# Optimization experiments

Hardware: AMD Instinct MI355X
Metric: run time of the kernel (lower is better)

Reference implementation:

```python
import jax, jax.numpy as jnp
import numpy as np

B, T = 16, 512
LAT, ACT, TSK = 512, 64, 96
E, NH, HD = 1024, 16, 64
L, HID, MAXS = 4, 4096, 512


def setup_inputs() -> dict:
    key = jax.random.key(0)
    ks = jax.random.split(key, 16)
    def rn(k, shape, std=0.02):
        return jax.random.normal(k, shape, jnp.float32) * std
    return {
        "z": jax.random.normal(ks[0], (B, T, LAT), jnp.float32),
        "a": jax.random.normal(ks[1], (B, T, ACT), jnp.float32),
        "task_emb": jax.random.normal(ks[2], (B, T, TSK), jnp.float32),
        "input_proj_w": rn(ks[3], (LAT + ACT + TSK, E)),
        "input_proj_b": jnp.zeros((E,), jnp.float32),
        "pos_emb": rn(ks[4], (1, MAXS, E)),
        "ln1_w": jnp.ones((L, E), jnp.float32),
        "ln1_b": jnp.zeros((L, E), jnp.float32),
        "qkv_w": rn(ks[5], (L, E, 3 * E)),
        "proj_w": rn(ks[6], (L, E, E)),
        "proj_b": jnp.zeros((L, E), jnp.float32),
        "ln2_w": jnp.ones((L, E), jnp.float32),
        "ln2_b": jnp.zeros((L, E), jnp.float32),
        "mlp_w1": rn(ks[7], (L, E, HID)),
        "mlp_b1": jnp.zeros((L, HID), jnp.float32),
        "mlp_w2": rn(ks[8], (L, HID, E)),
        "mlp_b2": jnp.zeros((L, E), jnp.float32),
        "out_norm_w": jnp.ones((E,), jnp.float32),
        "out_norm_b": jnp.zeros((E,), jnp.float32),
        "delta_w": rn(ks[9], (E, LAT)),
        "delta_b": jnp.zeros((LAT,), jnp.float32),
    }


def _ln(x, w, b, eps=1e-5):
    mu = jnp.mean(x, -1, keepdims=True)
    var = jnp.mean((x - mu) ** 2, -1, keepdims=True)
    return (x - mu) * jax.lax.rsqrt(var + eps) * w + b


def reference(z, a, task_emb, input_proj_w, input_proj_b, pos_emb,
              ln1_w, ln1_b, qkv_w, proj_w, proj_b, ln2_w, ln2_b,
              mlp_w1, mlp_b1, mlp_w2, mlp_b2,
              out_norm_w, out_norm_b, delta_w, delta_b):
    Bv, Tv, _ = z.shape
    x = jnp.concatenate([z, a, task_emb], axis=-1) @ input_proj_w + input_proj_b
    x = x + pos_emb[:, :Tv]
    scale = HD ** -0.5
    causal = jnp.tril(jnp.ones((Tv, Tv), bool))  # seq_start=0, no cache
    for l in range(L):
        h = _ln(x, ln1_w[l], ln1_b[l])
        qkv = (h @ qkv_w[l]).reshape(Bv, Tv, 3, NH, HD)
        q = jnp.swapaxes(qkv[:, :, 0], 1, 2) * scale  # (B,H,T,D)
        k = jnp.swapaxes(qkv[:, :, 1], 1, 2)
        v = jnp.swapaxes(qkv[:, :, 2], 1, 2)
        attn = jnp.einsum('bhqd,bhkd->bhqk', q, k)
        attn = jnp.where(causal, attn, -jnp.inf)
        attn = jax.nn.softmax(attn, axis=-1)
        o = jnp.einsum('bhqk,bhkd->bhqd', attn, v)
        o = jnp.swapaxes(o, 1, 2).reshape(Bv, Tv, E)
        x = x + (o @ proj_w[l] + proj_b[l])
        h2 = _ln(x, ln2_w[l], ln2_b[l])
        mid = jax.nn.gelu(h2 @ mlp_w1[l] + mlp_b1[l], approximate=False)
        x = x + (mid @ mlp_w2[l] + mlp_b2[l])
    x = _ln(x, out_norm_w, out_norm_b)
    return z + (x @ delta_w + delta_b)
```

## Files before the change

kernel.cpp:

```cpp
#include <hip/hip_runtime.h>
#include <hip/hip_bf16.h>
#include <math.h>

typedef unsigned short u16;
typedef unsigned int u32;
typedef __attribute__((ext_vector_type(4))) float f32x4;
typedef __attribute__((ext_vector_type(8))) short bf16x8;

#define DEV static __device__ __forceinline__

DEV u16 f2bf(float f) {
  __hip_bfloat16 h = __float2bfloat16(f);
  union { __hip_bfloat16 h; u16 u; } c; c.h = h; return c.u;
}

DEV void gload16(const void* g, void* l) {
  __builtin_amdgcn_global_load_lds((const __attribute__((address_space(1))) u32*)g,
                                   (__attribute__((address_space(3))) u32*)l, 16, 0, 0);
}

__global__ void transpose_w(const float* __restrict__ src, u16* __restrict__ dst,
                            int R, int C, int Rp) {
  __shared__ float tile[32][33];
  int tx = threadIdx.x, ty = threadIdx.y;
  int c0 = blockIdx.x * 32, r0 = blockIdx.y * 32;
  #pragma unroll
  for (int j = 0; j < 4; j++) {
    int r = r0 + ty + j * 8, c = c0 + tx;
    tile[ty + j * 8][tx] = (r < R && c < C) ? src[(size_t)r * C + c] : 0.f;
  }
  __syncthreads();
  #pragma unroll
  for (int j = 0; j < 4; j++) {
    int cc = c0 + ty + j * 8;
    int rr = r0 + tx;
    if (cc < C && rr < Rp) dst[(size_t)cc * Rp + rr] = f2bf(tile[tx][ty + j * 8]);
  }
}

__global__ void concat_k(const float* __restrict__ z, const float* __restrict__ a,
                         const float* __restrict__ te, u16* __restrict__ A) {
  const int total = 8192 * 704;
  for (int idx = blockIdx.x * 256 + threadIdx.x; idx < total; idx += gridDim.x * 256) {
    int m = idx / 704;
    int j = idx - m * 704;
    float v = 0.f;
// ... 76 lines not shown
  for (int l = 0; l < LB; l++) {
    int c = l * 512 + tid, rw = c >> 2, g = (c & 3) ^ ((rw >> 1) & 3);
    boff[l] = rw * Krow + g * 16;
  }
  const int ra = wr * (FM * 16) + (lane & 15);
  const int aRd = ra * 64 + (((lane >> 4) ^ ((ra >> 1) & 3)) << 4);
  const int rb = wc * 64 + (lane & 15);
  const int bRd = rb * 64 + (((lane >> 4) ^ ((rb >> 1) & 3)) << 4);

  f32x4 zero4 = {0.f, 0.f, 0.f, 0.f};
  f32x4 acc[FM][4];
  #pragma unroll
  for (int m = 0; m < FM; m++)
    #pragma unroll
    for (int n = 0; n < 4; n++) acc[m][n] = zero4;

  auto stageA = [&](int s) {
    char* Ad = lds + (s & 3) * SLICE;
    const char* src = Ag + (size_t)s * 64;
    #pragma unroll
    for (int l = 0; l < LA; l++)
      gload16(src + aoff[l], Ad + (l * 512 + w * 64) * 16);
  };
  auto stageB = [&](int s) {
    char* Bd = lds + (s & 3) * SLICE + ABYTES;
    const char* src = Bg + (size_t)s * 64;
    #pragma unroll
    for (int l = 0; l < LB; l++)
      gload16(src + boff[l], Bd + (l * 512 + w * 64) * 16);
  };

  const int NS = K >> 5;
  stageA(0); stageB(0); stageA(1); stageB(1);
  if constexpr (FM == 8) asm volatile("s_waitcnt vmcnt(4)" ::: "memory");
  else                   asm volatile("s_waitcnt vmcnt(3)" ::: "memory");
  __builtin_amdgcn_s_barrier();

  #pragma unroll 1
  for (int s = 0; s < NS; s++) {
    char* Ar = lds + (s & 3) * SLICE;
    char* Br = Ar + ABYTES;
    const bool pre = (s + 2 < NS);
    bf16x8 bfr[4], af[4];
    if constexpr (FM == 8) {
      #pragma unroll
      for (int n = 0; n < 4; n++) bfr[n] = *(const bf16x8*)(Br + bRd + n * 1024);
      #pragma unroll
      for (int m = 0; m < 4; m++) af[m] = *(const bf16x8*)(Ar + aRd + m * 1024);
      if (pre) stageA(s + 2);
      __builtin_amdgcn_sched_barrier(0);
      __builtin_amdgcn_s_barrier();
      asm volatile("s_waitcnt lgkmcnt(0)" ::: "memory");
      __builtin_amdgcn_sched_barrier(0);
      __builtin_amdgcn_s_setprio(1);
      #pragma unroll
      for (int m = 0; m < 4; m++)
        #pragma unroll
        for (int n = 0; n < 4; n++)
          acc[m][n] = __builtin_amdgcn_mfma_f32_16x16x32_bf16(af[m], bfr[n], acc[m][n], 0, 0, 0);
      __builtin_amdgcn_s_setprio(0);
      __builtin_amdgcn_sched_barrier(0);
      __builtin_amdgcn_s_barrier();
      #pragma unroll
      for (int m = 0; m < 4; m++) af[m] = *(const bf16x8*)(Ar + aRd + 4096 + m * 1024);
      if (pre) stageB(s + 2);
      __builtin_amdgcn_sched_barrier(0);
      __builtin_amdgcn_s_barrier();
      asm volatile("s_waitcnt lgkmcnt(0)" ::: "memory");
      __builtin_amdgcn_sched_barrier(0);
      __builtin_amdgcn_s_setprio(1);
      #pragma unroll
      for (int m = 0; m < 4; m++)
        #pragma unroll
        for (int n = 0; n < 4; n++)
          acc[4 + m][n] = __builtin_amdgcn_mfma_f32_16x16x32_bf16(af[m], bfr[n], acc[4 + m][n], 0, 0, 0);
      __builtin_amdgcn_s_setprio(0);
      __builtin_amdgcn_sched_barrier(0);
      if (pre) asm volatile("s_waitcnt vmcnt(4)" ::: "memory");
      else     asm volatile("s_waitcnt vmcnt(0)" ::: "memory");
      __builtin_amdgcn_s_barrier();
    } else {
      #pragma unroll
      for (int n = 0; n < 4; n++) bfr[n] = *(const bf16x8*)(Br + bRd + n * 1024);
      #pragma unroll
      for (int m = 0; m < 4; m++) af[m] = *(const bf16x8*)(Ar + aRd + m * 1024);
      if (pre) { stageA(s + 2); stageB(s + 2); }
      __builtin_amdgcn_sched_barrier(0);
      __builtin_amdgcn_s_barrier();
      asm volatile("s_waitcnt lgkmcnt(0)" ::: "memory");
      __builtin_amdgcn_sched_barrier(0);
      __builtin_amdgcn_s_setprio(1);
      #pragma unroll
      for (int m = 0; m < 4; m++)
        #pragma unroll
        for (int n = 0; n < 4; n++)
          acc[m][n] = __builtin_amdgcn_mfma_f32_16x16x32_bf16(af[m], bfr[n], acc[m][n], 0, 0, 0);
      __builtin_amdgcn_s_setprio(0);
      __builtin_amdgcn_sched_barrier(0);
      if (pre) asm volatile("s_waitcnt vmcnt(3)" ::: "memory");
      else     asm volatile("s_waitcnt vmcnt(0)" ::: "memory");
      __builtin_amdgcn_s_barrier();
    }
  }

  #pragma unroll
  for (int m = 0; m < FM; m++) {
    #pragma unroll
    for (int i = 0; i < 4; i++) {
      int gm = m0 + wr * (FM * 16) + m * 16 + ((lane >> 4) << 2) + i;
      #pragma unroll
      for (int n = 0; n < 4; n++) {
        int gn = n0 + wc * 64 + n * 16 + (lane & 15);
        float v = acc[m][n][i];
        if (EPI & 1) v += bias[gn];
        if (EPI & 2) v += pos[(size_t)(gm & 511) * N + gn];
        if (EPI & 4) v += res[(size_t)gm * N + gn];
        if (EPI & 8) v = 0.5f * v * (1.f + erff(v * 0.70710678118654752f));
        if (EPI & 16) outH[(size_t)gm * N + gn] = f2bf(v);
        else outF[(size_t)gm * N + gn] = v;
      }
    }
  }
}

__global__ __launch_bounds__(512) void attn_k(const u16* __restrict__ qkv,
                                              u16* __restrict__ o) {
  __shared__ u16 Ks[512 * 64];
  __shared__ u16 Vt[64 * 512];
  __shared__ u16 Ps[8 * 512];
  const int tid = threadIdx.x, lane = tid & 63, w = tid >> 6;
  const int b = blockIdx.x >> 4, h = blockIdx.x & 15;
  const u16* base = qkv + (size_t)b * 512 * 3072 + h * 64;

  #pragma unroll
  for (int it = 0; it < 8; it++) {
    int chunk = it * 512 + tid;
    int row = chunk >> 3;
    int ib = (chunk & 7) * 16;
    int lb = ib ^ ((row & 7) << 4);
    gload16((const char*)(base + 1024 + (size_t)row * 3072) + lb,
            (char*)Ks + (it * 512 + w * 64) * 16);
  }
  {
    const u16* vrow = base + 2048 + (size_t)tid * 3072;
    #pragma unroll
    for (int c = 0; c < 8; c++) {
      uint4 u = *(const uint4*)(vrow + c * 8);
      u32 vals[4] = {u.x, u.y, u.z, u.w};
      #pragma unroll
      for (int pcompo = 0; pcompo < 4; pcompo++) {
        int d0 = c * 8 + pcompo * 2;
        size_t by0 = ((size_t)d0 * 1024 + tid * 2) ^ (size_t)((d0 & 7) << 4);
        size_t by1 = ((size_t)(d0 + 1) * 1024 + tid * 2) ^ (size_t)(((d0 + 1) & 7) << 4);
        *(u16*)((char*)Vt + by0) = (u16)(vals[pcompo] & 0xffff);
        *(u16*)((char*)Vt + by1) = (u16)(vals[pcompo] >> 16);
      }
// ... 132 lines not shown
  };
  u16* wt_in   = (u16*)alloc((size_t)1024 * 704 * 2);
  u16* wt_qkv  = (u16*)alloc((size_t)4 * 3072 * 1024 * 2);
  u16* wt_proj = (u16*)alloc((size_t)4 * 1024 * 1024 * 2);
  u16* wt_m1   = (u16*)alloc((size_t)4 * 4096 * 1024 * 2);
  u16* wt_m2   = (u16*)alloc((size_t)4 * 1024 * 4096 * 2);
  u16* wt_d    = (u16*)alloc((size_t)512 * 1024 * 2);
  u16* abuf    = (u16*)alloc((size_t)8192 * 704 * 2);
  float* xbuf  = (float*)alloc((size_t)8192 * 1024 * 4);
  u16* hbuf    = (u16*)alloc((size_t)8192 * 1024 * 2);
  u16* big     = (u16*)alloc((size_t)8192 * 4096 * 2);
  u16* obuf    = (u16*)alloc((size_t)8192 * 1024 * 2);
  u16* qkvb = big;
  u16* mid  = big;

  dim3 tb(32, 8);
  auto TR = [&](const float* s, u16* d, int R, int C, int Rp) {
    dim3 g((C + 31) / 32, (Rp + 31) / 32);
    transpose_w<<<g, tb, 0, stream>>>(s, d, R, C, Rp);
  };
  TR(ipw, wt_in, 672, 1024, 704);
  for (int l = 0; l < 4; l++) TR(qkvw + (size_t)l * 1024 * 3072, wt_qkv + (size_t)l * 3072 * 1024, 1024, 3072, 1024);
  for (int l = 0; l < 4; l++) TR(projw + (size_t)l * 1024 * 1024, wt_proj + (size_t)l * 1024 * 1024, 1024, 1024, 1024);
  for (int l = 0; l < 4; l++) TR(w1 + (size_t)l * 1024 * 4096, wt_m1 + (size_t)l * 4096 * 1024, 1024, 4096, 1024);
  for (int l = 0; l < 4; l++) TR(w2 + (size_t)l * 4096 * 1024, wt_m2 + (size_t)l * 1024 * 4096, 4096, 1024, 4096);
  TR(dw, wt_d, 1024, 512, 1024);

  concat_k<<<4096, 256, 0, stream>>>(z, a, te, abuf);

  gemm8<4, 3><<<4 * 64, 512, 0, stream>>>(abuf, wt_in, xbuf, nullptr, ipb, nullptr, pos, 8192, 1024, 704, 4);

  for (int l = 0; l < 4; l++) {
    ln_k<<<2048, 256, 0, stream>>>(xbuf, ln1w + l * 1024, ln1b + l * 1024, hbuf);
    gemm8<8, 16><<<12 * 32, 512, 0, stream>>>(hbuf, wt_qkv + (size_t)l * 3072 * 1024, nullptr, qkvb, nullptr, nullptr, nullptr, 8192, 3072, 1024, 12);
    attn_k<<<256, 512, 0, stream>>>(qkvb, obuf);
    gemm8<4, 5><<<4 * 64, 512, 0, stream>>>(obuf, wt_proj + (size_t)l * 1024 * 1024, xbuf, nullptr, projb + l * 1024, xbuf, nullptr, 8192, 1024, 1024, 4);
    ln_k<<<2048, 256, 0, stream>>>(xbuf, ln2w + l * 1024, ln2b + l * 1024, hbuf);
    gemm8<8, 25><<<16 * 32, 512, 0, stream>>>(hbuf, wt_m1 + (size_t)l * 4096 * 1024, nullptr, mid, b1 + l * 4096, nullptr, nullptr, 8192, 4096, 1024, 16);
    gemm8<4, 5><<<4 * 64, 512, 0, stream>>>(mid, wt_m2 + (size_t)l * 1024 * 4096, xbuf, nullptr, b2 + l * 1024, xbuf, nullptr, 8192, 1024, 4096, 4);
  }
  ln_k<<<2048, 256, 0, stream>>>(xbuf, onw, onb, hbuf);
  gemm8<4, 5><<<2 * 64, 512, 0, stream>>>(hbuf, wt_d, out, nullptr, db, z, nullptr, 8192, 512, 1024, 2);
}
```

Baseline: 1.548 ms.

## Add new pipelined GEMM kernel with K-halved stages and XCD-aware tile mapping

Adds a gemmP kernel that splits each 64-wide K tile into two 32-wide halves in double-buffered LDS. It interleaves LDS reads, global-to-LDS prefetches and MFMA phases at a finer grain, and remaps block IDs so that consecutive tiles land on the same XCD. All the main transformer GEMMs now use this kernel, and gemm8 is reduced to its FM=4 path, which only the input projection still uses. The aim is to hide global load latency better and improve L2 locality. In exchange it adds more barriers per K step and uses a larger LDS footprint, which may lower occupancy.

```diff
diff --git a/kernel.cpp b/kernel.cpp
--- a/kernel.cpp
+++ b/kernel.cpp
@@ -154,8 +154,7 @@
 
   const int NS = K >> 5;
   stageA(0); stageB(0); stageA(1); stageB(1);
-  if constexpr (FM == 8) asm volatile("s_waitcnt vmcnt(4)" ::: "memory");
-  else                   asm volatile("s_waitcnt vmcnt(3)" ::: "memory");
+  asm volatile("s_waitcnt vmcnt(3)" ::: "memory");
   __builtin_amdgcn_s_barrier();
 
   #pragma unroll 1
@@ -164,65 +163,26 @@
     char* Br = Ar + ABYTES;
     const bool pre = (s + 2 < NS);
     bf16x8 bfr[4], af[4];
-    if constexpr (FM == 8) {
-      #pragma unroll
-      for (int n = 0; n < 4; n++) bfr[n] = *(const bf16x8*)(Br + bRd + n * 1024);
-      #pragma unroll
-      for (int m = 0; m < 4; m++) af[m] = *(const bf16x8*)(Ar + aRd + m * 1024);
-      if (pre) stageA(s + 2);
-      __builtin_amdgcn_sched_barrier(0);
-      __builtin_amdgcn_s_barrier();
-      asm volatile("s_waitcnt lgkmcnt(0)" ::: "memory");
-      __builtin_amdgcn_sched_barrier(0);
-      __builtin_amdgcn_s_setprio(1);
-      #pragma unroll
-      for (int m = 0; m < 4; m++)
-        #pragma unroll
-        for (int n = 0; n < 4; n++)
-          acc[m][n] = __builtin_amdgcn_mfma_f32_16x16x32_bf16(af[m], bfr[n], acc[m][n], 0, 0, 0);
-      __builtin_amdgcn_s_setprio(0);
-      __builtin_amdgcn_sched_barrier(0);
-      __builtin_amdgcn_s_barrier();
-      #pragma unroll
-      for (int m = 0; m < 4; m++) af[m] = *(const bf16x8*)(Ar + aRd + 4096 + m * 1024);
-      if (pre) stageB(s + 2);
-      __builtin_amdgcn_sched_barrier(0);
-      __builtin_amdgcn_s_barrier();
-      asm volatile("s_waitcnt lgkmcnt(0)" ::: "memory");
-      __builtin_amdgcn_sched_barrier(0);
-      __builtin_amdgcn_s_setprio(1);
-      #pragma unroll
-      for (int m = 0; m < 4; m++)
-        #pragma unroll
-        for (int n = 0; n < 4; n++)
-          acc[4 + m][n] = __builtin_amdgcn_mfma_f32_16x16x32_bf16(af[m], bfr[n], acc[4 + m][n], 0, 0, 0);
-      __builtin_amdgcn_s_setprio(0);
-      __builtin_amdgcn_sched_barrier(0);
-      if (pre) asm volatile("s_waitcnt vmcnt(4)" ::: "memory");
-      else     asm volatile("s_waitcnt vmcnt(0)" ::: "memory");
-      __builtin_amdgcn_s_barrier();
-    } else {
-      #pragma unroll
-      for (int n = 0; n < 4; n++) bfr[n] = *(const bf16x8*)(Br + bRd + n * 1024);
-      #pragma unroll
-      for (int m = 0; m < 4; m++) af[m] = *(const bf16x8*)(Ar + aRd + m * 1024);
-      if (pre) { stageA(s + 2); stageB(s + 2); }
-      __builtin_amdgcn_sched_barrier(0);
-      __builtin_amdgcn_s_barrier();
-      asm volatile("s_waitcnt lgkmcnt(0)" ::: "memory");
-      __builtin_amdgcn_sched_barrier(0);
-      __builtin_amdgcn_s_setprio(1);
-      #pragma unroll
-      for (int m = 0; m < 4; m++)
-        #pragma unroll
-        for (int n = 0; n < 4; n++)
-          acc[m][n] = __builtin_amdgcn_mfma_f32_16x16x32_bf16(af[m], bfr[n], acc[m][n], 0, 0, 0);
-      __builtin_amdgcn_s_setprio(0);
-      __builtin_amdgcn_sched_barrier(0);
-      if (pre) asm volatile("s_waitcnt vmcnt(3)" ::: "memory");
-      else     asm volatile("s_waitcnt vmcnt(0)" ::: "memory");
-      __builtin_amdgcn_s_barrier();
-    }
+    #pragma unroll
+    for (int n = 0; n < 4; n++) bfr[n] = *(const bf16x8*)(Br + bRd + n * 1024);
+    #pragma unroll
+    for (int m = 0; m < 4; m++) af[m] = *(const bf16x8*)(Ar + aRd + m * 1024);
+    if (pre) { stageA(s + 2); stageB(s + 2); }
+    __builtin_amdgcn_sched_barrier(0);
+    __builtin_amdgcn_s_barrier();
+    asm volatile("s_waitcnt lgkmcnt(0)" ::: "memory");
+    __builtin_amdgcn_sched_barrier(0);
+    __builtin_amdgcn_s_setprio(1);
+    #pragma unroll
+    for (int m = 0; m < 4; m++)
+      #pragma unroll
+      for (int n = 0; n < 4; n++)
+        acc[m][n] = __builtin_amdgcn_mfma_f32_16x16x32_bf16(af[m], bfr[n], acc[m][n], 0, 0, 0);
+    __builtin_amdgcn_s_setprio(0);
+    __builtin_amdgcn_sched_barrier(0);
+    if (pre) asm volatile("s_waitcnt vmcnt(3)" ::: "memory");
+    else     asm volatile("s_waitcnt vmcnt(0)" ::: "memory");
+    __builtin_amdgcn_s_barrier();
   }
 
   #pragma unroll
@@ -244,6 +204,198 @@
     }
   }
 }
+
+#define PHASE_MID \
+  __builtin_amdgcn_sched_barrier(0); \
+  __builtin_amdgcn_s_barrier(); \
+  asm volatile("s_waitcnt lgkmcnt(0)" ::: "memory"); \
+  __builtin_amdgcn_sched_barrier(0); \
+  __builtin_amdgcn_s_setprio(1);
+
+#define PHASE_END \
+  __builtin_amdgcn_s_setprio(0); \
+  __builtin_amdgcn_sched_barrier(0); \
+  __builtin_amdgcn_s_barrier();
+
+template <int FM, int EPI>
+__global__ __launch_bounds__(512, 2) void gemmP(
+    const u16* __restrict__ A, const u16* __restrict__ BT,
+    float* __restrict__ outF, u16* __restrict__ outH,
+    const float* __restrict__ bias, const float* __restrict__ res,
+    const float* __restrict__ pos, int M, int N, int K, int gx) {
+  constexpr int BM = FM * 32;
+  constexpr int ARB = BM * 64;
+  constexpr int BRB = 256 * 64;
+  constexpr int ABYT = 4 * ARB;
+  constexpr int LA = BM / 128;
+  __shared__ char lds[ABYT + 4 * BRB];
+
+  const int tid = threadIdx.x, lane = tid & 63, w = tid >> 6;
+  const int wr = w >> 2, wc = w & 3;
+
+  const int nwg = gridDim.x, orig = blockIdx.x;
+  const int q = nwg >> 3, r = nwg & 7;
+  const int xcd = orig & 7, loc = orig >> 3;
+  const int sid = (xcd < r ? xcd * (q + 1) : r * (q + 1) + (xcd - r) * q) + loc;
+  const int m0 = (sid / gx) * BM, n0 = (sid % gx) * 256;
+
+  const char* Ag = (const char*)(A + (size_t)m0 * K);
+  const char* Bg = (const char*)(BT + (size_t)n0 * K);
+  const int K2 = K * 2;
+  const int NT = K >> 6, NTm1 = NT - 1, NI = NT >> 1;
+
+  int aRd[FM], bRd[4];
+  #pragma unroll
+  for (int m = 0; m < FM; m++) {
+    int rr = wr * (FM * 16) + m * 16 + (lane & 15);
+    aRd[m] = rr * 64 + (((lane >> 4) ^ ((rr >> 1) & 3)) << 4);
+  }
+  #pragma unroll
+  for (int n = 0; n < 4; n++) {
+    int rr = wc * 64 + n * 16 + (lane & 15);
+    bRd[n] = rr * 64 + (((lane >> 4) ^ ((rr >> 1) & 3)) << 4);
+  }
+  int asrc[LA], adst[LA], bsrc[2], bdst[2];
+  #pragma unroll
+  for (int l = 0; l < LA; l++) {
+    int c = l * 512 + tid, rw = c >> 2, sl = c & 3;
+    asrc[l] = rw * K2 + ((sl ^ ((rw >> 1) & 3)) << 4);
+    adst[l] = c * 16;
+  }
+  #pragma unroll
+  for (int l = 0; l < 2; l++) {
+    int c = l * 512 + tid, rw = c >> 2, sl = c & 3;
+    bsrc[l] = rw * K2 + ((sl ^ ((rw >> 1) & 3)) << 4);
+    bdst[l] = c * 16;
+  }
+
+  auto stA = [&](int tau, int kh) {
+    char* d = lds + ((tau & 1) * 2 + kh) * ARB;
+    const char* s = Ag + (size_t)(tau < NT ? tau : NTm1) * 128 + kh * 64;
+    #pragma unroll
+    for (int l = 0; l < LA; l++) gload16(s + asrc[l], d + adst[l]);
+  };
+  auto stB = [&](int tau, int kh) {
+    char* d = lds + ABYT + ((tau & 1) * 2 + kh) * BRB;
+    const char* s = Bg + (size_t)(tau < NT ? tau : NTm1) * 128 + kh * 64;
+    #pragma unroll
+    for (int l = 0; l < 2; l++) gload16(s + bsrc[l], d + bdst[l]);
+  };
+
+  f32x4 zero4 = {0.f, 0.f, 0.f, 0.f};
+  f32x4 acc[FM][4];
+  #pragma unroll
+  for (int m = 0; m < FM; m++)
+    #pragma unroll
+    for (int n = 0; n < 4; n++) acc[m][n] = zero4;
+
+  bf16x8 afr[4], bfr[4];
+  auto rdA4 = [&](int buf, int kh, int mb) {
+    const char* base = lds + (buf * 2 + kh) * ARB;
+    #pragma unroll
+    for (int mm = 0; mm < 4; mm++) afr[mm] = *(const bf16x8*)(base + aRd[mb + mm]);
+  };
+  auto rdB4 = [&](int buf, int kh) {
+    const char* base = lds + ABYT + (buf * 2 + kh) * BRB;
+    #pragma unroll
+    for (int nn = 0; nn < 4; nn++) bfr[nn] = *(const bf16x8*)(base + bRd[nn]);
+  };
+
+#define MFMA16(MB) \
+  _Pragma("unroll") \
+  for (int mm = 0; mm < 4; mm++) \
+    _Pragma("unroll") \
+    for (int nn = 0; nn < 4; nn++) \
+      acc[(MB) + mm][nn] = __builtin_amdgcn_mfma_f32_16x16x32_bf16(afr[mm], bfr[nn], acc[(MB) + mm][nn], 0, 0, 0);
+
+  if constexpr (FM == 8) {
+    stA(0, 0); stB(0, 0); stA(0, 1); stB(0, 1); stA(1, 0); stB(1, 0); stB(1, 1);
+    asm volatile("s_waitcnt vmcnt(8)" ::: "memory");
+  } else {
+    stA(0, 0); stB(0, 0); stA(0, 1); stB(0, 1); stA(1, 0); stB(1, 0);
+    asm volatile("s_waitcnt vmcnt(3)" ::: "memory");
+  }
+  __builtin_amdgcn_s_barrier();
+
+  #pragma unroll 1
+  for (int J = 0; J < NI; J++) {
+    const int t = 2 * J;
+    if constexpr (FM == 8) {
+      asm volatile("s_waitcnt vmcnt(8)" ::: "memory");
+      __builtin_amdgcn_sched_barrier(0);
+      rdB4(0, 0); rdA4(0, 0, 0); stA(t + 1, 1);
+      PHASE_MID; MFMA16(0); PHASE_END;
+      asm volatile("s_waitcnt vmcnt(8)" ::: "memory");
+      __builtin_amdgcn_sched_barrier(0);
+      rdA4(0, 0, 4); stB(t + 2, 0);
+      PHASE_MID; MFMA16(4); PHASE_END;
+      asm volatile("s_waitcnt vmcnt(8)" ::: "memory");
+      __builtin_amdgcn_sched_barrier(0);
+      rdB4(0, 1); rdA4(0, 1, 0); stA(t + 2, 0);
+      PHASE_MID; MFMA16(0); PHASE_END;
+      asm volatile("s_waitcnt vmcnt(8)" ::: "memory");
+      __builtin_amdgcn_sched_barrier(0);
+      rdA4(0, 1, 4); stB(t + 2, 1);
+      PHASE_MID; MFMA16(4); PHASE_END;
+      asm volatile("s_waitcnt vmcnt(8)" ::: "memory");
+      __builtin_amdgcn_sched_barrier(0);
+      rdB4(1, 0); rdA4(1, 0, 0); stA(t + 2, 1);
+      PHASE_MID; MFMA16(0); PHASE_END;
+      asm volatile("s_waitcnt vmcnt(8)" ::: "memory");
+      __builtin_amdgcn_sched_barrier(0);
+      rdA4(1, 0, 4); stB(t + 3, 0);
+      PHASE_MID; MFMA16(4); PHASE_END;
+      asm volatile("s_waitcnt vmcnt(8)" ::: "memory");
+      __builtin_amdgcn_sched_barrier(0);
+      rdB4(1, 1); rdA4(1, 1, 0); stA(t + 3, 0);
+      PHASE_MID; MFMA16(0); PHASE_END;
+      asm volatile("s_waitcnt vmcnt(8)" ::: "memory");
+      __builtin_amdgcn_sched_barrier(0);
+      rdA4(1, 1, 4); stB(t + 3, 1);
+      PHASE_MID; MFMA16(4); PHASE_END;
+    } else {
+      asm volatile("s_waitcnt vmcnt(3)" ::: "memory");
+      __builtin_amdgcn_sched_barrier(0);
+      rdB4(0, 0); rdA4(0, 0, 0); stA(t + 1, 1); stB(t + 1, 1);
+      PHASE_MID; MFMA16(0); PHASE_END;
+      asm volatile("s_waitcnt vmcnt(3)" ::: "memory");
+      __builtin_amdgcn_sched_barrier(0);
+      rdB4(0, 1); rdA4(0, 1, 0); stA(t + 2, 0); stB(t + 2, 0);
+      PHASE_MID; MFMA16(0); PHASE_END;
+      asm volatile("s_waitcnt vmcnt(3)" ::: "memory");
+      __builtin_amdgcn_sched_barrier(0);
+      rdB4(1, 0); rdA4(1, 0, 0); stA(t + 2, 1); stB(t + 2, 1);
+      PHASE_MID; MFMA16(0); PHASE_END;
+      asm volatile("s_waitcnt vmcnt(3)" ::: "memory");
+      __builtin_amdgcn_sched_barrier(0);
+      rdB4(1, 1); rdA4(1, 1, 0); stA(t + 3, 0); stB(t + 3, 0);
+      PHASE_MID; MFMA16(0); PHASE_END;
+    }
+  }
+  asm volatile("s_waitcnt vmcnt(0)" ::: "memory");
+
+  #pragma unroll
+  for (int m = 0; m < FM; m++) {
+    #pragma unroll
+    for (int i = 0; i < 4; i++) {
+      int gm = m0 + wr * (FM * 16) + m * 16 + ((lane >> 4) << 2) + i;
+      #pragma unroll
+      for (int n = 0; n < 4; n++) {
+        int gn = n0 + wc * 64 + n * 16 + (lane & 15);
+        float v = acc[m][n][i];
+        if (EPI & 1) v += bias[gn];
+        if (EPI & 2) v += pos[(size_t)(gm & 511) * N + gn];
+        if (EPI & 4) v += res[(size_t)gm * N + gn];
+        if (EPI & 8) v = 0.5f * v * (1.f + erff(v * 0.70710678118654752f));
+        if (EPI & 16) outH[(size_t)gm * N + gn] = f2bf(v);
+        else outF[(size_t)gm * N + gn] = v;
+      }
+    }
+  }
+}
+#undef MFMA16
+#undef PHASE_MID
+#undef PHASE_END
 
 __global__ __launch_bounds__(512) void attn_k(const u16* __restrict__ qkv,
                                               u16* __restrict__ o) {
@@ -442,13 +594,13 @@
 
   for (int l = 0; l < 4; l++) {
     ln_k<<<2048, 256, 0, stream>>>(xbuf, ln1w + l * 1024, ln1b + l * 1024, hbuf);
-    gemm8<8, 16><<<12 * 32, 512, 0, stream>>>(hbuf, wt_qkv + (size_t)l * 3072 * 1024, nullptr, qkvb, nullptr, nullptr, nullptr, 8192, 3072, 1024, 12);
+    gemmP<8, 16><<<384, 512, 0, stream>>>(hbuf, wt_qkv + (size_t)l * 3072 * 1024, nullptr, qkvb, nullptr, nullptr, nullptr, 8192, 3072, 1024, 12);
     attn_k<<<256, 512, 0, stream>>>(qkvb, obuf);
-    gemm8<4, 5><<<4 * 64, 512, 0, stream>>>(obuf, wt_proj + (size_t)l * 1024 * 1024, xbuf, nullptr, projb + l * 1024, xbuf, nullptr, 8192, 1024, 1024, 4);
+    gemmP<4, 5><<<256, 512, 0, stream>>>(obuf, wt_proj + (size_t)l * 1024 * 1024, xbuf, nullptr, projb + l * 1024, xbuf, nullptr, 8192, 1024, 1024, 4);
     ln_k<<<2048, 256, 0, stream>>>(xbuf, ln2w + l * 1024, ln2b + l * 1024, hbuf);
-    gemm8<8, 25><<<16 * 32, 512, 0, stream>>>(hbuf, wt_m1 + (size_t)l * 4096 * 1024, nullptr, mid, b1 + l * 4096, nullptr, nullptr, 8192, 4096, 1024, 16);
-    gemm8<4, 5><<<4 * 64, 512, 0, stream>>>(mid, wt_m2 + (size_t)l * 1024 * 4096, xbuf, nullptr, b2 + l * 1024, xbuf, nullptr, 8192, 1024, 4096, 4);
+    gemmP<8, 25><<<512, 512, 0, stream>>>(hbuf, wt_m1 + (size_t)l * 4096 * 1024, nullptr, mid, b1 + l * 4096, nullptr, nullptr, 8192, 4096, 1024, 16);
+    gemmP<4, 5><<<256, 512, 0, stream>>>(mid, wt_m2 + (size_t)l * 1024 * 4096, xbuf, nullptr, b2 + l * 1024, xbuf, nullptr, 8192, 1024, 4096, 4);
   }
   ln_k<<<2048, 256, 0, stream>>>(xbuf, onw, onb, hbuf);
-  gemm8<4, 5><<<2 * 64, 512, 0, stream>>>(hbuf, wt_d, out, nullptr, db, z, nullptr, 8192, 512, 1024, 2);
-}
+  gemmP<4, 5><<<128, 512, 0, stream>>>(hbuf, wt_d, out, nullptr, db, z, nullptr, 8192, 512, 1024, 2);
+}
```

Measured after the change: 1.542 ms. Within noise of the previous version (-0.4%).

## Add ping-pong pipelined GEMM with 64-wide K tiles and XCD-aware tile remap

Applied to the files above, without the earlier changes.

Adds a new gemmP kernel that stages 64-wide K slices into double-buffered LDS regions and splits each iteration into several phases. Each phase issues an LDS read and a global prefetch, then a barrier and an MFMA block, so memory traffic overlaps compute more finely. It also remaps block IDs across the 8 XCDs so neighbouring tiles share L2, and sets launch bounds to two workgroups per CU. All layer GEMMs and the output GEMM switch to gemmP, and the old gemm8 keeps only its single-phase path, which now serves just the input projection. The cost is more barriers per K step and a larger LDS footprint, which may limit occupancy.

```diff
diff --git a/kernel.cpp b/kernel.cpp
--- a/kernel.cpp
+++ b/kernel.cpp
@@ -154,8 +154,7 @@
 
   const int NS = K >> 5;
   stageA(0); stageB(0); stageA(1); stageB(1);
-  if constexpr (FM == 8) asm volatile("s_waitcnt vmcnt(4)" ::: "memory");
-  else                   asm volatile("s_waitcnt vmcnt(3)" ::: "memory");
+  asm volatile("s_waitcnt vmcnt(3)" ::: "memory");
   __builtin_amdgcn_s_barrier();
 
   #pragma unroll 1
@@ -164,65 +163,26 @@
     char* Br = Ar + ABYTES;
     const bool pre = (s + 2 < NS);
     bf16x8 bfr[4], af[4];
-    if constexpr (FM == 8) {
-      #pragma unroll
-      for (int n = 0; n < 4; n++) bfr[n] = *(const bf16x8*)(Br + bRd + n * 1024);
-      #pragma unroll
-      for (int m = 0; m < 4; m++) af[m] = *(const bf16x8*)(Ar + aRd + m * 1024);
-      if (pre) stageA(s + 2);
-      __builtin_amdgcn_sched_barrier(0);
-      __builtin_amdgcn_s_barrier();
-      asm volatile("s_waitcnt lgkmcnt(0)" ::: "memory");
-      __builtin_amdgcn_sched_barrier(0);
-      __builtin_amdgcn_s_setprio(1);
-      #pragma unroll
-      for (int m = 0; m < 4; m++)
-        #pragma unroll
-        for (int n = 0; n < 4; n++)
-          acc[m][n] = __builtin_amdgcn_mfma_f32_16x16x32_bf16(af[m], bfr[n], acc[m][n], 0, 0, 0);
-      __builtin_amdgcn_s_setprio(0);
-      __builtin_amdgcn_sched_barrier(0);
-      __builtin_amdgcn_s_barrier();
-      #pragma unroll
-      for (int m = 0; m < 4; m++) af[m] = *(const bf16x8*)(Ar + aRd + 4096 + m * 1024);
-      if (pre) stageB(s + 2);
-      __builtin_amdgcn_sched_barrier(0);
-      __builtin_amdgcn_s_barrier();
-      asm volatile("s_waitcnt lgkmcnt(0)" ::: "memory");
-      __builtin_amdgcn_sched_barrier(0);
-      __builtin_amdgcn_s_setprio(1);
-      #pragma unroll
-      for (int m = 0; m < 4; m++)
-        #pragma unroll
-        for (int n = 0; n < 4; n++)
-          acc[4 + m][n] = __builtin_amdgcn_mfma_f32_16x16x32_bf16(af[m], bfr[n], acc[4 + m][n], 0, 0, 0);
-      __builtin_amdgcn_s_setprio(0);
-      __builtin_amdgcn_sched_barrier(0);
-      if (pre) asm volatile("s_waitcnt vmcnt(4)" ::: "memory");
-      else     asm volatile("s_waitcnt vmcnt(0)" ::: "memory");
-      __builtin_amdgcn_s_barrier();
-    } else {
-      #pragma unroll
-      for (int n = 0; n < 4; n++) bfr[n] = *(const bf16x8*)(Br + bRd + n * 1024);
-      #pragma unroll
-      for (int m = 0; m < 4; m++) af[m] = *(const bf16x8*)(Ar + aRd + m * 1024);
-      if (pre) { stageA(s + 2); stageB(s + 2); }
-      __builtin_amdgcn_sched_barrier(0);
-      __builtin_amdgcn_s_barrier();
-      asm volatile("s_waitcnt lgkmcnt(0)" ::: "memory");
-      __builtin_amdgcn_sched_barrier(0);
-      __builtin_amdgcn_s_setprio(1);
-      #pragma unroll
-      for (int m = 0; m < 4; m++)
-        #pragma unroll
-        for (int n = 0; n < 4; n++)
-          acc[m][n] = __builtin_amdgcn_mfma_f32_16x16x32_bf16(af[m], bfr[n], acc[m][n], 0, 0, 0);
-      __builtin_amdgcn_s_setprio(0);
-      __builtin_amdgcn_sched_barrier(0);
-      if (pre) asm volatile("s_waitcnt vmcnt(3)" ::: "memory");
-      else     asm volatile("s_waitcnt vmcnt(0)" ::: "memory");
-      __builtin_amdgcn_s_barrier();
-    }
+    #pragma unroll
+    for (int n = 0; n < 4; n++) bfr[n] = *(const bf16x8*)(Br + bRd + n * 1024);
+    #pragma unroll
+    for (int m = 0; m < 4; m++) af[m] = *(const bf16x8*)(Ar + aRd + m * 1024);
+    if (pre) { stageA(s + 2); stageB(s + 2); }
+    __builtin_amdgcn_sched_barrier(0);
+    __builtin_amdgcn_s_barrier();
+    asm volatile("s_waitcnt lgkmcnt(0)" ::: "memory");
+    __builtin_amdgcn_sched_barrier(0);
+    __builtin_amdgcn_s_setprio(1);
+    #pragma unroll
+    for (int m = 0; m < 4; m++)
+      #pragma unroll
+      for (int n = 0; n < 4; n++)
+        acc[m][n] = __builtin_amdgcn_mfma_f32_16x16x32_bf16(af[m], bfr[n], acc[m][n], 0, 0, 0);
+    __builtin_amdgcn_s_setprio(0);
+    __builtin_amdgcn_sched_barrier(0);
+    if (pre) asm volatile("s_waitcnt vmcnt(3)" ::: "memory");
+    else     asm volatile("s_waitcnt vmcnt(0)" ::: "memory");
+    __builtin_amdgcn_s_barrier();
   }
 
   #pragma unroll
@@ -244,6 +204,190 @@
     }
   }
 }
+
+#define SB0 __builtin_amdgcn_sched_barrier(0)
+#define VMW(N) asm volatile("s_waitcnt vmcnt(" #N ")" ::: "memory")
+#define PH_TAIL(MFMAS) \
+  SB0; __builtin_amdgcn_s_barrier(); \
+  asm volatile("s_waitcnt lgkmcnt(0)" ::: "memory"); SB0; \
+  __builtin_amdgcn_s_setprio(1); MFMAS; __builtin_amdgcn_s_setprio(0); \
+  SB0; __builtin_amdgcn_s_barrier();
+#define PH_TAILV(MFMAS, NN) \
+  SB0; __builtin_amdgcn_s_barrier(); \
+  asm volatile("s_waitcnt lgkmcnt(0)" ::: "memory"); SB0; \
+  __builtin_amdgcn_s_setprio(1); MFMAS; __builtin_amdgcn_s_setprio(0); \
+  SB0; VMW(NN); __builtin_amdgcn_s_barrier();
+#define MM16(MB, BF) \
+  _Pragma("unroll") \
+  for (int mm = 0; mm < 4; mm++) \
+    _Pragma("unroll") \
+    for (int nn = 0; nn < 4; nn++) \
+      acc[(MB) + mm][nn] = __builtin_amdgcn_mfma_f32_16x16x32_bf16(afr[mm], BF[nn], acc[(MB) + mm][nn], 0, 0, 0);
+#define RD_A(BUF, K2L, MB) { \
+  const char* _b = aRdB[BUF]; \
+  afr[0] = *(const bf16x8*)(_b + aby[(MB) + 0][K2L]); \
+  afr[1] = *(const bf16x8*)(_b + aby[(MB) + 1][K2L]); \
+  afr[2] = *(const bf16x8*)(_b + aby[(MB) + 2][K2L]); \
+  afr[3] = *(const bf16x8*)(_b + aby[(MB) + 3][K2L]); }
+#define RD_BALL(BUF) { \
+  const char* _b = bRdB[BUF]; \
+  bfr0[0] = *(const bf16x8*)(_b + bby[0][0]); bfr1[0] = *(const bf16x8*)(_b + bby[0][1]); \
+  bfr0[1] = *(const bf16x8*)(_b + bby[1][0]); bfr1[1] = *(const bf16x8*)(_b + bby[1][1]); \
+  bfr0[2] = *(const bf16x8*)(_b + bby[2][0]); bfr1[2] = *(const bf16x8*)(_b + bby[2][1]); \
+  bfr0[3] = *(const bf16x8*)(_b + bby[3][0]); bfr1[3] = *(const bf16x8*)(_b + bby[3][1]); }
+
+template <int FM, int EPI>
+__global__ __launch_bounds__(512, 2) void gemmP(
+    const u16* __restrict__ A, const u16* __restrict__ BT,
+    float* __restrict__ outF, u16* __restrict__ outH,
+    const float* __restrict__ bias, const float* __restrict__ res,
+    const float* __restrict__ pos, int M, int N, int K, int gx) {
+  constexpr int RB = 16384;
+  constexpr int NAREG = (FM == 8 ? 4 : 2);
+  constexpr int BOFF = NAREG * RB;
+  __shared__ char lds[BOFF + 4 * RB];
+
+  const int tid = threadIdx.x, lane = tid & 63, w = tid >> 6;
+  const int wr = w >> 2, wc = w & 3;
+  const int ln = lane & 15, g = lane >> 4;
+
+  const int nwg = gridDim.x, orig = blockIdx.x;
+  const int q = nwg >> 3, r = nwg & 7;
+  const int xcd = orig & 7, loc = orig >> 3;
+  const int sid = (xcd < r ? xcd * (q + 1) : r * (q + 1) + (xcd - r) * q) + loc;
+  const int m0 = (sid / gx) * (FM * 32), n0 = (sid % gx) * 256;
+
+  const char* Ag = (const char*)(A + (size_t)m0 * K);
+  const char* Bg = (const char*)(BT + (size_t)n0 * K);
+  const size_t K2 = (size_t)K * 2;
+  const int NT = K >> 6, NTm1 = NT - 1, NI = NT >> 1;
+
+  int aby[FM][2], bby[4][2];
+  #pragma unroll
+  for (int m = 0; m < FM; m++) {
+    int rr = (FM == 8 ? 0 : wr * 64) + m * 16 + ln;
+    #pragma unroll
+    for (int k2 = 0; k2 < 2; k2++)
+      aby[m][k2] = rr * 128 + (((k2 * 4 + g) ^ (rr & 7)) << 4);
+  }
+  #pragma unroll
+  for (int n = 0; n < 4; n++) {
+    int rr = (wc & 1) * 64 + n * 16 + ln;
+    #pragma unroll
+    for (int k2 = 0; k2 < 2; k2++)
+      bby[n][k2] = rr * 128 + (((k2 * 4 + g) ^ (rr & 7)) << 4);
+  }
+  const char* aRdB[2];
+  const char* bRdB[2];
+  if constexpr (FM == 8) {
+    aRdB[0] = lds + (0 * 2 + wr) * RB;
+    aRdB[1] = lds + (1 * 2 + wr) * RB;
+  } else {
+    aRdB[0] = lds;
+    aRdB[1] = lds + RB;
+  }
+  bRdB[0] = lds + BOFF + (0 * 2 + (wc >> 1)) * RB;
+  bRdB[1] = lds + BOFF + (1 * 2 + (wc >> 1)) * RB;
+
+  int soff[2], sdst[2];
+  #pragma unroll
+  for (int l = 0; l < 2; l++) {
+    int c = l * 512 + tid, rw = c >> 3, sl = c & 7;
+    soff[l] = rw * (int)K2 + ((sl ^ (rw & 7)) << 4);
+    sdst[l] = (l * 512 + w * 64) * 16;
+  }
+
+  auto stA = [&](int buf, int tau, int h) {
+    char* d = lds + (FM == 8 ? (buf * 2 + h) : buf) * RB;
+    const char* s = Ag + (size_t)(tau < NT ? tau : NTm1) * 128 + (FM == 8 ? (size_t)h * 128 * K2 : 0);
+    #pragma unroll
+    for (int l = 0; l < 2; l++) gload16(s + soff[l], d + sdst[l]);
+  };
+  auto stB = [&](int buf, int tau, int gg) {
+    char* d = lds + BOFF + (buf * 2 + gg) * RB;
+    const char* s = Bg + (size_t)(tau < NT ? tau : NTm1) * 128 + (size_t)gg * 128 * K2;
+    #pragma unroll
+    for (int l = 0; l < 2; l++) gload16(s + soff[l], d + sdst[l]);
+  };
+
+  f32x4 zero4 = {0.f, 0.f, 0.f, 0.f};
+  f32x4 acc[FM][4];
+  #pragma unroll
+  for (int m = 0; m < FM; m++)
+    #pragma unroll
+    for (int n = 0; n < 4; n++) acc[m][n] = zero4;
+
+  bf16x8 afr[4], bfr0[4], bfr1[4];
+
+  if constexpr (FM == 8) {
+    stA(0, 0, 0); stA(0, 0, 1); stB(0, 0, 0); stB(0, 0, 1); stB(1, 1, 0); stB(1, 1, 1);
+    VMW(4);
+    __builtin_amdgcn_s_barrier();
+    #pragma unroll 1
+    for (int J = 0; J < NI; J++) {
+      const int t = 2 * J;
+      RD_BALL(0); RD_A(0, 0, 0); stA(1, t + 1, 0);
+      PH_TAIL(MM16(0, bfr0));
+      RD_A(0, 0, 4); stA(1, t + 1, 1); stB(0, t + 2, 0);
+      PH_TAIL(MM16(4, bfr0));
+      RD_A(0, 1, 0); stB(0, t + 2, 1);
+      PH_TAIL(MM16(0, bfr1));
+      RD_A(0, 1, 4);
+      PH_TAILV(MM16(4, bfr1), 4);
+      RD_BALL(1); RD_A(1, 0, 0); stA(0, t + 2, 0);
+      PH_TAIL(MM16(0, bfr0));
+      RD_A(1, 0, 4); stA(0, t + 2, 1);
+      PH_TAIL(MM16(4, bfr0));
+      RD_A(1, 1, 0); stB(1, t + 3, 0);
+      PH_TAIL(MM16(0, bfr1));
+      RD_A(1, 1, 4); stB(1, t + 3, 1);
+      PH_TAILV(MM16(4, bfr1), 4);
+    }
+  } else {
+    stA(0, 0, 0); stB(0, 0, 0); stB(0, 0, 1); stB(1, 1, 0); stB(1, 1, 1);
+    VMW(4);
+    __builtin_amdgcn_s_barrier();
+    #pragma unroll 1
+    for (int J = 0; J < NI; J++) {
+      const int t = 2 * J;
+      RD_BALL(0); RD_A(0, 0, 0); stA(1, t + 1, 0);
+      PH_TAIL(MM16(0, bfr0));
+      RD_A(0, 1, 0); stB(0, t + 2, 0);
+      PH_TAILV(MM16(0, bfr1), 2);
+      RD_BALL(1); RD_A(1, 0, 0); stB(0, t + 2, 1); stA(0, t + 2, 0);
+      PH_TAIL(MM16(0, bfr0));
+      RD_A(1, 1, 0); stB(1, t + 3, 0); stB(1, t + 3, 1);
+      PH_TAILV(MM16(0, bfr1), 4);
+    }
+  }
+  VMW(0);
+
+  #pragma unroll
+  for (int m = 0; m < FM; m++) {
+    #pragma unroll
+    for (int i = 0; i < 4; i++) {
+      int gm = m0 + wr * (FM * 16) + m * 16 + (g << 2) + i;
+      #pragma unroll
+      for (int n = 0; n < 4; n++) {
+        int gn = n0 + wc * 64 + n * 16 + ln;
+        float v = acc[m][n][i];
+        if (EPI & 1) v += bias[gn];
+        if (EPI & 2) v += pos[(size_t)(gm & 511) * N + gn];
+        if (EPI & 4) v += res[(size_t)gm * N + gn];
+        if (EPI & 8) v = 0.5f * v * (1.f + erff(v * 0.70710678118654752f));
+        if (EPI & 16) outH[(size_t)gm * N + gn] = f2bf(v);
+        else outF[(size_t)gm * N + gn] = v;
+      }
+    }
+  }
+}
+#undef RD_BALL
+#undef RD_A
+#undef MM16
+#undef PH_TAILV
+#undef PH_TAIL
+#undef VMW
+#undef SB0
 
 __global__ __launch_bounds__(512) void attn_k(const u16* __restrict__ qkv,
                                               u16* __restrict__ o) {
@@ -442,13 +586,13 @@
 
   for (int l = 0; l < 4; l++) {
     ln_k<<<2048, 256, 0, stream>>>(xbuf, ln1w + l * 1024, ln1b + l * 1024, hbuf);
-    gemm8<8, 16><<<12 * 32, 512, 0, stream>>>(hbuf, wt_qkv + (size_t)l * 3072 * 1024, nullptr, qkvb, nullptr, nullptr, nullptr, 8192, 3072, 1024, 12);
+    gemmP<8, 16><<<384, 512, 0, stream>>>(hbuf, wt_qkv + (size_t)l * 3072 * 1024, nullptr, qkvb, nullptr, nullptr, nullptr, 8192, 3072, 1024, 12);
     attn_k<<<256, 512, 0, stream>>>(qkvb, obuf);
-    gemm8<4, 5><<<4 * 64, 512, 0, stream>>>(obuf, wt_proj + (size_t)l * 1024 * 1024, xbuf, nullptr, projb + l * 1024, xbuf, nullptr, 8192, 1024, 1024, 4);
+    gemmP<4, 5><<<256, 512, 0, stream>>>(obuf, wt_proj + (size_t)l * 1024 * 1024, xbuf, nullptr, projb + l * 1024, xbuf, nullptr, 8192, 1024, 1024, 4);
     ln_k<<<2048, 256, 0, stream>>>(xbuf, ln2w + l * 1024, ln2b + l * 1024, hbuf);
-    gemm8<8, 25><<<16 * 32, 512, 0, stream>>>(hbuf, wt_m1 + (size_t)l * 4096 * 1024, nullptr, mid, b1 + l * 4096, nullptr, nullptr, 8192, 4096, 1024, 16);
-    gemm8<4, 5><<<4 * 64, 512, 0, stream>>>(mid, wt_m2 + (size_t)l * 1024 * 4096, xbuf, nullptr, b2 + l * 1024, xbuf, nullptr, 8192, 1024, 4096, 4);
+    gemmP<8, 25><<<512, 512, 0, stream>>>(hbuf, wt_m1 + (size_t)l * 4096 * 1024, nullptr, mid, b1 + l * 4096, nullptr, nullptr, 8192, 4096, 1024, 16);
+    gemmP<4, 5><<<256, 512, 0, stream>>>(mid, wt_m2 + (size_t)l * 1024 * 4096, xbuf, nullptr, b2 + l * 1024, xbuf, nullptr, 8192, 1024, 4096, 4);
   }
   ln_k<<<2048, 256, 0, stream>>>(xbuf, onw, onb, hbuf);
-  gemm8<4, 5><<<2 * 64, 512, 0, stream>>>(hbuf, wt_d, out, nullptr, db, z, nullptr, 8192, 512, 1024, 2);
-}
+  gemmP<4, 5><<<128, 512, 0, stream>>>(hbuf, wt_d, out, nullptr, db, z, nullptr, 8192, 512, 1024, 2);
+}
```

After: 1.452 ms. -6.2%, faster.

## Add triple-buffered 128x256 GEMM kernel with XCD-aware tile mapping and fast GELU

Applied to the files above, without the earlier changes.

Introduces a new gemmT kernel that uses 128x256 output tiles, K-steps of 64, and a three-stage LDS ring with swizzled layout. It remaps block IDs so contiguous tiles land on the same XCD, and it replaces all per-layer GEMMs and the final delta GEMM with this kernel. It also swaps the erf-based GELU for a sigmoid/tanh-style approximation, and it removes the FM==8 path from the old gemm8. The goals are better latency hiding, better L2 locality, and a cheaper epilogue. The cost is GELU accuracy and higher LDS use, at about 144KB per block.

```diff
diff --git a/kernel.cpp b/kernel.cpp
--- a/kernel.cpp
+++ b/kernel.cpp
@@ -12,6 +12,11 @@
 DEV u16 f2bf(float f) {
   __hip_bfloat16 h = __float2bfloat16(f);
   union { __hip_bfloat16 h; u16 u; } c; c.h = h; return c.u;
+}
+
+DEV float fast_gelu(float v) {
+  float u = v * (1.5957691216f + 0.0713548162f * v * v);
+  return v * __builtin_amdgcn_rcpf(1.f + __expf(-u));
 }
 
 DEV void gload16(const void* g, void* l) {
@@ -154,8 +159,7 @@
 
   const int NS = K >> 5;
   stageA(0); stageB(0); stageA(1); stageB(1);
-  if constexpr (FM == 8) asm volatile("s_waitcnt vmcnt(4)" ::: "memory");
-  else                   asm volatile("s_waitcnt vmcnt(3)" ::: "memory");
+  asm volatile("s_waitcnt vmcnt(3)" ::: "memory");
   __builtin_amdgcn_s_barrier();
 
   #pragma unroll 1
@@ -164,65 +168,26 @@
     char* Br = Ar + ABYTES;
     const bool pre = (s + 2 < NS);
     bf16x8 bfr[4], af[4];
-    if constexpr (FM == 8) {
-      #pragma unroll
-      for (int n = 0; n < 4; n++) bfr[n] = *(const bf16x8*)(Br + bRd + n * 1024);
-      #pragma unroll
-      for (int m = 0; m < 4; m++) af[m] = *(const bf16x8*)(Ar + aRd + m * 1024);
-      if (pre) stageA(s + 2);
-      __builtin_amdgcn_sched_barrier(0);
-      __builtin_amdgcn_s_barrier();
-      asm volatile("s_waitcnt lgkmcnt(0)" ::: "memory");
-      __builtin_amdgcn_sched_barrier(0);
-      __builtin_amdgcn_s_setprio(1);
-      #pragma unroll
-      for (int m = 0; m < 4; m++)
-        #pragma unroll
-        for (int n = 0; n < 4; n++)
-          acc[m][n] = __builtin_amdgcn_mfma_f32_16x16x32_bf16(af[m], bfr[n], acc[m][n], 0, 0, 0);
-      __builtin_amdgcn_s_setprio(0);
-      __builtin_amdgcn_sched_barrier(0);
-      __builtin_amdgcn_s_barrier();
-      #pragma unroll
-      for (int m = 0; m < 4; m++) af[m] = *(const bf16x8*)(Ar + aRd + 4096 + m * 1024);
-      if (pre) stageB(s + 2);
-      __builtin_amdgcn_sched_barrier(0);
-      __builtin_amdgcn_s_barrier();
-      asm volatile("s_waitcnt lgkmcnt(0)" ::: "memory");
-      __builtin_amdgcn_sched_barrier(0);
-      __builtin_amdgcn_s_setprio(1);
-      #pragma unroll
-      for (int m = 0; m < 4; m++)
-        #pragma unroll
-        for (int n = 0; n < 4; n++)
-          acc[4 + m][n] = __builtin_amdgcn_mfma_f32_16x16x32_bf16(af[m], bfr[n], acc[4 + m][n], 0, 0, 0);
-      __builtin_amdgcn_s_setprio(0);
-      __builtin_amdgcn_sched_barrier(0);
-      if (pre) asm volatile("s_waitcnt vmcnt(4)" ::: "memory");
-      else     asm volatile("s_waitcnt vmcnt(0)" ::: "memory");
-      __builtin_amdgcn_s_barrier();
-    } else {
-      #pragma unroll
-      for (int n = 0; n < 4; n++) bfr[n] = *(const bf16x8*)(Br + bRd + n * 1024);
-      #pragma unroll
-      for (int m = 0; m < 4; m++) af[m] = *(const bf16x8*)(Ar + aRd + m * 1024);
-      if (pre) { stageA(s + 2); stageB(s + 2); }
-      __builtin_amdgcn_sched_barrier(0);
-      __builtin_amdgcn_s_barrier();
-      asm volatile("s_waitcnt lgkmcnt(0)" ::: "memory");
-      __builtin_amdgcn_sched_barrier(0);
-      __builtin_amdgcn_s_setprio(1);
-      #pragma unroll
-      for (int m = 0; m < 4; m++)
-        #pragma unroll
-        for (int n = 0; n < 4; n++)
-          acc[m][n] = __builtin_amdgcn_mfma_f32_16x16x32_bf16(af[m], bfr[n], acc[m][n], 0, 0, 0);
-      __builtin_amdgcn_s_setprio(0);
-      __builtin_amdgcn_sched_barrier(0);
-      if (pre) asm volatile("s_waitcnt vmcnt(3)" ::: "memory");
-      else     asm volatile("s_waitcnt vmcnt(0)" ::: "memory");
-      __builtin_amdgcn_s_barrier();
-    }
+    #pragma unroll
+    for (int n = 0; n < 4; n++) bfr[n] = *(const bf16x8*)(Br + bRd + n * 1024);
+    #pragma unroll
+    for (int m = 0; m < 4; m++) af[m] = *(const bf16x8*)(Ar + aRd + m * 1024);
+    if (pre) { stageA(s + 2); stageB(s + 2); }
+    __builtin_amdgcn_sched_barrier(0);
+    __builtin_amdgcn_s_barrier();
+    asm volatile("s_waitcnt lgkmcnt(0)" ::: "memory");
+    __builtin_amdgcn_sched_barrier(0);
+    __builtin_amdgcn_s_setprio(1);
+    #pragma unroll
+    for (int m = 0; m < 4; m++)
+      #pragma unroll
+      for (int n = 0; n < 4; n++)
+        acc[m][n] = __builtin_amdgcn_mfma_f32_16x16x32_bf16(af[m], bfr[n], acc[m][n], 0, 0, 0);
+    __builtin_amdgcn_s_setprio(0);
+    __builtin_amdgcn_sched_barrier(0);
+    if (pre) asm volatile("s_waitcnt vmcnt(3)" ::: "memory");
+    else     asm volatile("s_waitcnt vmcnt(0)" ::: "memory");
+    __builtin_amdgcn_s_barrier();
   }
 
   #pragma unroll
@@ -237,13 +202,153 @@
         if (EPI & 1) v += bias[gn];
         if (EPI & 2) v += pos[(size_t)(gm & 511) * N + gn];
         if (EPI & 4) v += res[(size_t)gm * N + gn];
-        if (EPI & 8) v = 0.5f * v * (1.f + erff(v * 0.70710678118654752f));
+        if (EPI & 8) v = fast_gelu(v);
         if (EPI & 16) outH[(size_t)gm * N + gn] = f2bf(v);
         else outF[(size_t)gm * N + gn] = v;
       }
     }
   }
 }
+
+#define SB0 __builtin_amdgcn_sched_barrier(0)
+template <int EPI>
+__global__ __launch_bounds__(512, 2) void gemmT(
+    const u16* __restrict__ A, const u16* __restrict__ BT,
+    float* __restrict__ outF, u16* __restrict__ outH,
+    const float* __restrict__ bias, const float* __restrict__ res,
+    const float* __restrict__ pos, int M, int N, int K, int gx) {
+  constexpr int RB = 16384;
+  constexpr int BUF = 3 * RB;
+  __shared__ char lds[3 * BUF];
+
+  const int tid = threadIdx.x, lane = tid & 63, w = tid >> 6;
+  const int wr = w >> 2, wc = w & 3;
+  const int ln = lane & 15, g = lane >> 4;
+
+  const int nwg = gridDim.x, orig = blockIdx.x;
+  const int q = nwg >> 3, r = nwg & 7;
+  const int xcd = orig & 7, loc = orig >> 3;
+  const int sid = (xcd < r ? xcd * (q + 1) : r * (q + 1) + (xcd - r) * q) + loc;
+  const int m0 = (sid / gx) * 128, n0 = (sid % gx) * 256;
+
+  const char* Ag = (const char*)(A + (size_t)m0 * K);
+  const char* Bg = (const char*)(BT + (size_t)n0 * K);
+  const size_t K2 = (size_t)K * 2;
+  const int NT = K >> 6, NTm1 = NT - 1;
+
+  int aby[4][2], bby[4][2];
+  #pragma unroll
+  for (int m = 0; m < 4; m++) {
+    int rr = wr * 64 + m * 16 + ln;
+    #pragma unroll
+    for (int k2 = 0; k2 < 2; k2++)
+      aby[m][k2] = rr * 128 + (((k2 * 4 + g) ^ (rr & 7)) << 4);
+  }
+  #pragma unroll
+  for (int n = 0; n < 4; n++) {
+    int rr = (wc & 1) * 64 + n * 16 + ln;
+    #pragma unroll
+    for (int k2 = 0; k2 < 2; k2++)
+      bby[n][k2] = rr * 128 + (((k2 * 4 + g) ^ (rr & 7)) << 4);
+  }
+  const int bsel = RB + (wc >> 1) * RB;
+
+  int soff[2], sdst[2];
+  #pragma unroll
+  for (int l = 0; l < 2; l++) {
+    int c = l * 512 + tid, rw = c >> 3, sl = c & 7;
+    soff[l] = rw * (int)K2 + ((sl ^ (rw & 7)) << 4);
+    sdst[l] = (l * 512 + w * 64) * 16;
+  }
+
+  auto stT = [&](int buf, int tau) {
+    int tt = tau < NT ? tau : NTm1;
+    char* base = lds + buf * BUF;
+    const char* sa  = Ag + (size_t)tt * 128;
+    const char* sb0 = Bg + (size_t)tt * 128;
+    const char* sb1 = sb0 + (size_t)128 * K2;
+    #pragma unroll
+    for (int l = 0; l < 2; l++) gload16(sa  + soff[l], base + sdst[l]);
+    #pragma unroll
+    for (int l = 0; l < 2; l++) gload16(sb0 + soff[l], base + RB + sdst[l]);
+    #pragma unroll
+    for (int l = 0; l < 2; l++) gload16(sb1 + soff[l], base + 2 * RB + sdst[l]);
+  };
+
+  f32x4 zero4 = {0.f, 0.f, 0.f, 0.f};
+  f32x4 acc[4][4];
+  #pragma unroll
+  for (int m = 0; m < 4; m++)
+    #pragma unroll
+    for (int n = 0; n < 4; n++) acc[m][n] = zero4;
+
+  bf16x8 afr[4][2], bfr0[4], bfr1[4];
+
+  stT(0, 0); stT(1, 1);
+
+  int b0 = 0, b1 = 1, b2 = 2;
+  #pragma unroll 1
+  for (int t = 0; t < NT; t++) {
+    asm volatile("s_waitcnt vmcnt(6)" ::: "memory");
+    SB0;
+    __builtin_amdgcn_s_barrier();
+    stT(b2, t + 2);
+    const char* ab = lds + b0 * BUF;
+    const char* bb = ab + bsel;
+    #pragma unroll
+    for (int n = 0; n < 4; n++) bfr0[n] = *(const bf16x8*)(bb + bby[n][0]);
+    #pragma unroll
+    for (int m = 0; m < 4; m++) afr[m][0] = *(const bf16x8*)(ab + aby[m][0]);
+    SB0;
+    #pragma unroll
+    for (int n = 0; n < 4; n++) bfr1[n] = *(const bf16x8*)(bb + bby[n][1]);
+    #pragma unroll
+    for (int m = 0; m < 4; m++) afr[m][1] = *(const bf16x8*)(ab + aby[m][1]);
+    SB0;
+    asm volatile("s_waitcnt lgkmcnt(8)" ::: "memory");
+    SB0;
+    __builtin_amdgcn_s_setprio(1);
+    #pragma unroll
+    for (int m = 0; m < 4; m++)
+      #pragma unroll
+      for (int n = 0; n < 4; n++)
+        acc[m][n] = __builtin_amdgcn_mfma_f32_16x16x32_bf16(afr[m][0], bfr0[n], acc[m][n], 0, 0, 0);
+    __builtin_amdgcn_s_setprio(0);
+    SB0;
+    asm volatile("s_waitcnt lgkmcnt(0)" ::: "memory");
+    SB0;
+    __builtin_amdgcn_s_setprio(1);
+    #pragma unroll
+    for (int m = 0; m < 4; m++)
+      #pragma unroll
+      for (int n = 0; n < 4; n++)
+        acc[m][n] = __builtin_amdgcn_mfma_f32_16x16x32_bf16(afr[m][1], bfr1[n], acc[m][n], 0, 0, 0);
+    __builtin_amdgcn_s_setprio(0);
+    SB0;
+    int tmp = b0; b0 = b1; b1 = b2; b2 = tmp;
+  }
+  asm volatile("s_waitcnt vmcnt(0)" ::: "memory");
+
+  #pragma unroll
+  for (int m = 0; m < 4; m++) {
+    #pragma unroll
+    for (int i = 0; i < 4; i++) {
+      int gm = m0 + wr * 64 + m * 16 + (g << 2) + i;
+      #pragma unroll
+      for (int n = 0; n < 4; n++) {
+        int gn = n0 + wc * 64 + n * 16 + ln;
+        float v = acc[m][n][i];
+        if (EPI & 1) v += bias[gn];
+        if (EPI & 2) v += pos[(size_t)(gm & 511) * N + gn];
+        if (EPI & 4) v += res[(size_t)gm * N + gn];
+        if (EPI & 8) v = fast_gelu(v);
+        if (EPI & 16) outH[(size_t)gm * N + gn] = f2bf(v);
+        else outF[(size_t)gm * N + gn] = v;
+      }
+    }
+  }
+}
+#undef SB0
 
 __global__ __launch_bounds__(512) void attn_k(const u16* __restrict__ qkv,
                                               u16* __restrict__ o) {
@@ -442,13 +547,13 @@
 
   for (int l = 0; l < 4; l++) {
     ln_k<<<2048, 256, 0, stream>>>(xbuf, ln1w + l * 1024, ln1b + l * 1024, hbuf);
-    gemm8<8, 16><<<12 * 32, 512, 0, stream>>>(hbuf, wt_qkv + (size_t)l * 3072 * 1024, nullptr, qkvb, nullptr, nullptr, nullptr, 8192, 3072, 1024, 12);
+    gemmT<16><<<768, 512, 0, stream>>>(hbuf, wt_qkv + (size_t)l * 3072 * 1024, nullptr, qkvb, nullptr, nullptr, nullptr, 8192, 3072, 1024, 12);
     attn_k<<<256, 512, 0, stream>>>(qkvb, obuf);
-    gemm8<4, 5><<<4 * 64, 512, 0, stream>>>(obuf, wt_proj + (size_t)l * 1024 * 1024, xbuf, nullptr, projb + l * 1024, xbuf, nullptr, 8192, 1024, 1024, 4);
+    gemmT<5><<<256, 512, 0, stream>>>(obuf, wt_proj + (size_t)l * 1024 * 1024, xbuf, nullptr, projb + l * 1024, xbuf, nullptr, 8192, 1024, 1024, 4);
     ln_k<<<2048, 256, 0, stream>>>(xbuf, ln2w + l * 1024, ln2b + l * 1024, hbuf);
-    gemm8<8, 25><<<16 * 32, 512, 0, stream>>>(hbuf, wt_m1 + (size_t)l * 4096 * 1024, nullptr, mid, b1 + l * 4096, nullptr, nullptr, 8192, 4096, 1024, 16);
-    gemm8<4, 5><<<4 * 64, 512, 0, stream>>>(mid, wt_m2 + (size_t)l * 1024 * 4096, xbuf, nullptr, b2 + l * 1024, xbuf, nullptr, 8192, 1024, 4096, 4);
+    gemmT<25><<<1024, 512, 0, stream>>>(hbuf, wt_m1 + (size_t)l * 4096 * 1024, nullptr, mid, b1 + l * 4096, nullptr, nullptr, 8192, 4096, 1024, 16);
+    gemmT<5><<<256, 512, 0, stream>>>(mid, wt_m2 + (size_t)l * 1024 * 4096, xbuf, nullptr, b2 + l * 1024, xbuf, nullptr, 8192, 1024, 4096, 4);
   }
   ln_k<<<2048, 256, 0, stream>>>(xbuf, onw, onb, hbuf);
-  gemm8<4, 5><<<2 * 64, 512, 0, stream>>>(hbuf, wt_d, out, nullptr, db, z, nullptr, 8192, 512, 1024, 2);
-}
+  gemmT<5><<<128, 512, 0, stream>>>(hbuf, wt_d, out, nullptr, db, z, nullptr, 8192, 512, 1024, 2);
+}
```

New measurement: 1.435 ms. 7.3% less time.
